# Kernel tuning notes

Measured on AMD Instinct MI355X. Metric: run time of the kernel, lower is better.

## Reference

```python
import jax, jax.numpy as jnp
import numpy as np
from jax import lax

# static config
P = 16          # patch_len
S = 8           # stride_base
MAX_OFF = 4.0


def setup_inputs() -> dict:
    key = jax.random.key(0)
    ks = jax.random.split(key, 7)
    B, L, N, A, D = 64, 512, 64, 64, 256
    x = jax.random.normal(ks[0], (B, L, N), dtype=jnp.float32)
    conv_w = jax.random.normal(ks[1], (32, N, 3), dtype=jnp.float32) * 0.05
    conv_b = jnp.zeros((32,), dtype=jnp.float32)
    lin_w = jax.random.normal(ks[2], (A, 32), dtype=jnp.float32) * 0.1
    lin_b = jnp.zeros((A,), dtype=jnp.float32)
    wp_w = jax.random.normal(ks[3], (D, P), dtype=jnp.float32) * 0.1
    wp_b = jnp.zeros((D,), dtype=jnp.float32)
    return {"x": x, "conv_w": conv_w, "conv_b": conv_b,
            "lin_w": lin_w, "lin_b": lin_b, "wp_w": wp_w, "wp_b": wp_b}


def _forward(x, conv_w, conv_b, lin_w, lin_b, wp_w, wp_b):
    B, L, N = x.shape
    A = lin_w.shape[0]
    D = wp_w.shape[0]
    z = jnp.transpose(x, (0, 2, 1))  # (B, N, L) -- channels = series

    # offset head: Conv1d(N->32, k=3, pad=1) -> ReLU -> global avg pool -> Linear(32->A)
    h = lax.conv_general_dilated(z, conv_w, window_strides=(1,),
                                 padding=[(1, 1)],
                                 dimension_numbers=("NCH", "OIH", "NCH"))
    h = jax.nn.relu(h + conv_b[None, :, None])      # (B, 32, L)
    pooled = jnp.mean(h, axis=-1)                    # (B, 32)
    delta = MAX_OFF * jnp.tanh(pooled @ lin_w.T + lin_b)  # (B, A)

    # sampling positions: anchor + offset + centered patch index, clamped to [0, L-1]
    anchors = jnp.arange(A, dtype=jnp.float32) * S
    pidx = jnp.arange(P, dtype=jnp.float32) - (P - 1) / 2.0
    xs = anchors[None, :, None] + delta[:, :, None] + pidx[None, None, :]  # (B, A, P)
    xs = jnp.clip(xs, 0.0, float(L - 1))

    # 1D bilinear gather (equivalent to grid_sample with y=0, border pad, align_corners=True)
    i0 = jnp.floor(xs).astype(jnp.int32)
    f = xs - i0.astype(xs.dtype)                     # (B, A, P)
    i1 = jnp.minimum(i0 + 1, L - 1)
    gather = jax.vmap(lambda zb, ib: zb[:, ib])      # (N,L),(A,P) -> (N,A,P)
    g0 = gather(z, i0)                               # (B, N, A, P)
    g1 = gather(z, i1)
    samp = g0 * (1.0 - f)[:, None] + g1 * f[:, None]  # (B, N, A, P)

    # patch projection W_P: (P -> D)
    out = jnp.einsum("bnap,dp->bnad", samp, wp_w) + wp_b  # (B, N, A, D)
    return out.reshape(B * N, A, D)


def reference(x, conv_w, conv_b, lin_w, lin_b, wp_w, wp_b):
    return _forward(x, conv_w, conv_b, lin_w, lin_b, wp_w, wp_b)
```

## Files before the change

kernel.cpp:

```cpp
#include <hip/hip_runtime.h>
#include <hip/hip_bf16.h>
#include <cmath>

#define BB 64
#define LL 512
#define NN 64
#define AA 64
#define PP 16
#define DD 256
#define MAX_OFF 4.0f
#define STRIDE_S 8

__global__ __launch_bounds__(256) void conv_pool_kernel(
    const float* __restrict__ x,
    const float* __restrict__ conv_w,
    const float* __restrict__ conv_b,
    float* __restrict__ pool_partial)
{
    const int c = blockIdx.x;
    const int b = blockIdx.y;
    const int t = threadIdx.x;

    __shared__ float4 wl[3 * 16 * 32];
    __shared__ float  xl[66 * 64];
    __shared__ float  red[8][32];

    for (int idx = t; idx < 1536; idx += 256) {
        int o  = idx & 31;
        int nv = (idx >> 5) & 15;
        int k  = idx >> 9;
        float4 v;
        v.x = conv_w[(o * 64 + nv * 4 + 0) * 3 + k];
        v.y = conv_w[(o * 64 + nv * 4 + 1) * 3 + k];
        v.z = conv_w[(o * 64 + nv * 4 + 2) * 3 + k];
        v.w = conv_w[(o * 64 + nv * 4 + 3) * 3 + k];
        wl[idx] = v;
    }

    const int base_row = c * 64 - 1;
    for (int idx = t; idx < 66 * 16; idx += 256) {
        int j  = idx >> 4;
        int nv = idx & 15;
        int row = base_row + j;
        float4 v = make_float4(0.f, 0.f, 0.f, 0.f);
        if (row >= 0 && row < LL)
            v = *reinterpret_cast<const float4*>(&x[((size_t)b * LL + row) * NN + nv * 4]);
        *reinterpret_cast<float4*>(&xl[j * 64 + nv * 4]) = v;
    }
    __syncthreads();

    const int o  = t & 31;
    const int lg = t >> 5;

    float s[8];
#pragma unroll
    for (int j = 0; j < 8; ++j) s[j] = 0.f;

#pragma unroll
    for (int nv = 0; nv < 16; ++nv) {
        float4 xv[10];
#pragma unroll
        for (int j = 0; j < 10; ++j)
            xv[j] = *reinterpret_cast<const float4*>(&xl[(lg * 8 + j) * 64 + nv * 4]);
#pragma unroll
        for (int k = 0; k < 3; ++k) {
            float4 w4 = wl[(k * 16 + nv) * 32 + o];
#pragma unroll
            for (int j = 0; j < 8; ++j) {
                s[j] = fmaf(xv[j + k].x, w4.x, s[j]);
                s[j] = fmaf(xv[j + k].y, w4.y, s[j]);
                s[j] = fmaf(xv[j + k].z, w4.z, s[j]);
                s[j] = fmaf(xv[j + k].w, w4.w, s[j]);
            }
        }
    }

    const float cb = conv_b[o];
    float part = 0.f;
#pragma unroll
    for (int j = 0; j < 8; ++j) part += fmaxf(s[j] + cb, 0.f);
    red[lg][o] = part;
    __syncthreads();

    if (t < 32) {
        float sum = 0.f;
#pragma unroll
        for (int g = 0; g < 8; ++g) sum += red[g][t];
        pool_partial[((size_t)b * 8 + c) * 32 + t] = sum;
    }
}

__global__ __launch_bounds__(64) void delta_kernel(
    const float* __restrict__ pool_partial,
    const float* __restrict__ lin_w,
    const float* __restrict__ lin_b,
    float* __restrict__ delta)
{
    const int b = blockIdx.x;
    const int t = threadIdx.x;
    __shared__ float pooled[32];

    if (t < 32) {
        float s = 0.f;
#pragma unroll
        for (int c = 0; c < 8; ++c) s += pool_partial[((size_t)b * 8 + c) * 32 + t];
        pooled[t] = s * (1.0f / 512.0f);
    }
    __syncthreads();

    float s = lin_b[t];
#pragma unroll
    for (int o = 0; o < 32; ++o) s = fmaf(pooled[o], lin_w[t * 32 + o], s);
    delta[b * AA + t] = MAX_OFF * tanhf(s);
}

#define XR_STRIDE 68

__global__ __launch_bounds__(256) void patch_proj_kernel(
    const float* __restrict__ x,
    const float* __restrict__ wp_w,
    const float* __restrict__ wp_b,
    const float* __restrict__ delta,
    float* __restrict__ out)
{
    const int a = blockIdx.x;
    const int b = blockIdx.y;
    const int t = threadIdx.x;

    __shared__ float xr[17 * XR_STRIDE];
    __shared__ float samp[64 * 16];

    const float dlt  = delta[b * AA + a];
    const float base = (float)(a * STRIDE_S) - 7.5f + dlt;
    const int   r0   = (int)floorf(base);

    for (int idx = t; idx < 17 * 16; idx += 256) {
        int j  = idx >> 4;
        int nv = idx & 15;
        int row = r0 + j;
        row = max(0, min(LL - 1, row));
        float4 v = *reinterpret_cast<const float4*>(&x[((size_t)b * LL + row) * NN + nv * 4]);
        *reinterpret_cast<float4*>(&xr[j * XR_STRIDE + nv * 4]) = v;
    }
    __syncthreads();

    {
        const int p = t & 15;
        float xs = base + (float)p;
        xs = fminf(fmaxf(xs, 0.f), (float)(LL - 1));
        int   i0 = (int)floorf(xs);
        float f  = xs - (float)i0;
        int   i1 = min(i0 + 1, LL - 1);
        const int j0 = i0 - r0;
        const int j1 = i1 - r0;
        const int nq = t >> 4;
#pragma unroll
        for (int i = 0; i < 4; ++i) {
            int n = nq + 16 * i;
            float g0 = xr[j0 * XR_STRIDE + n];
            float g1 = xr[j1 * XR_STRIDE + n];
            samp[n * 16 + p] = g0 + f * (g1 - g0);
        }
    }
    __syncthreads();

    const int dq = t & 63;
    const int ng = t >> 6;

    float w_[4][16];
#pragma unroll
    for (int r = 0; r < 4; ++r) {
#pragma unroll
        for (int pv = 0; pv < 4; ++pv) {
            float4 v = *reinterpret_cast<const float4*>(&wp_w[(dq * 4 + r) * 16 + pv * 4]);
            w_[r][pv * 4 + 0] = v.x;
            w_[r][pv * 4 + 1] = v.y;
            w_[r][pv * 4 + 2] = v.z;
            w_[r][pv * 4 + 3] = v.w;
        }
    }
    const float4 bias = *reinterpret_cast<const float4*>(&wp_b[dq * 4]);

#pragma unroll
    for (int i = 0; i < 16; ++i) {
        const int n = ng * 16 + i;
        const float4 s0 = *reinterpret_cast<const float4*>(&samp[n * 16 + 0]);
        const float4 s1 = *reinterpret_cast<const float4*>(&samp[n * 16 + 4]);
        const float4 s2 = *reinterpret_cast<const float4*>(&samp[n * 16 + 8]);
        const float4 s3 = *reinterpret_cast<const float4*>(&samp[n * 16 + 12]);
        float sp[16] = { s0.x, s0.y, s0.z, s0.w,  s1.x, s1.y, s1.z, s1.w,
                         s2.x, s2.y, s2.z, s2.w,  s3.x, s3.y, s3.z, s3.w };
        float acc0 = bias.x, acc1 = bias.y, acc2 = bias.z, acc3 = bias.w;
#pragma unroll
        for (int p = 0; p < 16; ++p) {
            const float s = sp[p];
            acc0 = fmaf(s, w_[0][p], acc0);
            acc1 = fmaf(s, w_[1][p], acc1);
            acc2 = fmaf(s, w_[2][p], acc2);
            acc3 = fmaf(s, w_[3][p], acc3);
        }
        const size_t row = ((size_t)(b * NN + n) * AA + a);
        float4 o4 = make_float4(acc0, acc1, acc2, acc3);
        *reinterpret_cast<float4*>(&out[row * DD + dq * 4]) = o4;
    }
}

extern "C" void kernel_launch(void* const* d_in, const int* in_sizes, int n_in,
                              void* d_out, int out_size, void* d_ws, size_t ws_size,
                              hipStream_t stream)
{
    const float* x      = (const float*)d_in[0];
    const float* conv_w = (const float*)d_in[1];
    const float* conv_b = (const float*)d_in[2];
    const float* lin_w  = (const float*)d_in[3];
    const float* lin_b  = (const float*)d_in[4];
    const float* wp_w   = (const float*)d_in[5];
    const float* wp_b   = (const float*)d_in[6];
    float* out = (float*)d_out;

    float* pool_partial = (float*)d_ws;
    float* delta        = pool_partial + 16384;

    conv_pool_kernel<<<dim3(8, BB), 256, 0, stream>>>(x, conv_w, conv_b, pool_partial);
    delta_kernel<<<BB, 64, 0, stream>>>(pool_partial, lin_w, lin_b, delta);
    patch_proj_kernel<<<dim3(AA, BB), 256, 0, stream>>>(x, wp_w, wp_b, delta, out);
}
```

Baseline: 74.08 us.

## Use bf16 MFMA for patch projection with zero-padded K

Replaces the scalar FP32 FMA patch projection with a bf16 MFMA 16x16x32 matrix multiply. Sampled values and projection weights are converted to bf16 in shared memory, with K padded from 16 to 32 using zeros. Output is now written as scalar stores strided across d instead of float4 stores. This lowers precision to bf16 and may hurt store coalescing, while the kernel is likely bound by output writes anyway.

```diff
diff --git a/kernel.cpp b/kernel.cpp
--- a/kernel.cpp
+++ b/kernel.cpp
@@ -10,6 +10,15 @@
 #define DD 256
 #define MAX_OFF 4.0f
 #define STRIDE_S 8
+
+typedef __attribute__((ext_vector_type(8))) short short8_t;
+typedef __attribute__((ext_vector_type(4))) float float4_t;
+
+static __device__ __forceinline__ unsigned short f2bf(float x) {
+    union { float f; unsigned u; } v; v.f = x;
+    unsigned r = (v.u + 0x7FFFu + ((v.u >> 16) & 1u)) >> 16;
+    return (unsigned short)r;
+}
 
 __global__ __launch_bounds__(256) void conv_pool_kernel(
     const float* __restrict__ x,
@@ -115,6 +124,8 @@
 }
 
 #define XR_STRIDE 68
+#define SA_STRIDE 40
+#define BW_STRIDE 24
 
 __global__ __launch_bounds__(256) void patch_proj_kernel(
     const float* __restrict__ x,
@@ -126,9 +137,14 @@
     const int a = blockIdx.x;
     const int b = blockIdx.y;
     const int t = threadIdx.x;
-
-    __shared__ float xr[17 * XR_STRIDE];
-    __shared__ float samp[64 * 16];
+    const int lane = t & 63;
+    const int w  = t >> 6;
+    const int lg = lane >> 4;
+    const int lr = lane & 15;
+
+    __shared__ float          xr[17 * XR_STRIDE];
+    __shared__ unsigned short sampA[64 * SA_STRIDE];
+    __shared__ unsigned short bw[256 * BW_STRIDE];
 
     const float dlt  = delta[b * AA + a];
     const float base = (float)(a * STRIDE_S) - 7.5f + dlt;
@@ -137,71 +153,90 @@
     for (int idx = t; idx < 17 * 16; idx += 256) {
         int j  = idx >> 4;
         int nv = idx & 15;
-        int row = r0 + j;
-        row = max(0, min(LL - 1, row));
+        int row = max(0, min(LL - 1, r0 + j));
         float4 v = *reinterpret_cast<const float4*>(&x[((size_t)b * LL + row) * NN + nv * 4]);
         *reinterpret_cast<float4*>(&xr[j * XR_STRIDE + nv * 4]) = v;
     }
+    for (int idx = t; idx < 256 * 8; idx += 256) {
+        int d  = idx >> 3;
+        int pp = idx & 7;
+        float2 v = *reinterpret_cast<const float2*>(&wp_w[d * 16 + pp * 2]);
+        unsigned pk = (unsigned)f2bf(v.x) | ((unsigned)f2bf(v.y) << 16);
+        *reinterpret_cast<unsigned*>(&bw[d * BW_STRIDE + pp * 2]) = pk;
+    }
+    for (int idx = t; idx < 64 * 8; idx += 256) {
+        int n  = idx >> 3;
+        int ww = idx & 7;
+        reinterpret_cast<unsigned*>(&sampA[n * SA_STRIDE])[8 + ww] = 0u;
+    }
     __syncthreads();
 
     {
-        const int p = t & 15;
-        float xs = base + (float)p;
-        xs = fminf(fmaxf(xs, 0.f), (float)(LL - 1));
-        int   i0 = (int)floorf(xs);
-        float f  = xs - (float)i0;
-        int   i1 = min(i0 + 1, LL - 1);
-        const int j0 = i0 - r0;
-        const int j1 = i1 - r0;
-        const int nq = t >> 4;
-#pragma unroll
-        for (int i = 0; i < 4; ++i) {
-            int n = nq + 16 * i;
-            float g0 = xr[j0 * XR_STRIDE + n];
-            float g1 = xr[j1 * XR_STRIDE + n];
-            samp[n * 16 + p] = g0 + f * (g1 - g0);
-        }
-    }
-    __syncthreads();
-
-    const int dq = t & 63;
-    const int ng = t >> 6;
-
-    float w_[4][16];
-#pragma unroll
-    for (int r = 0; r < 4; ++r) {
-#pragma unroll
-        for (int pv = 0; pv < 4; ++pv) {
-            float4 v = *reinterpret_cast<const float4*>(&wp_w[(dq * 4 + r) * 16 + pv * 4]);
-            w_[r][pv * 4 + 0] = v.x;
-            w_[r][pv * 4 + 1] = v.y;
-            w_[r][pv * 4 + 2] = v.z;
-            w_[r][pv * 4 + 3] = v.w;
-        }
-    }
-    const float4 bias = *reinterpret_cast<const float4*>(&wp_b[dq * 4]);
-
-#pragma unroll
-    for (int i = 0; i < 16; ++i) {
-        const int n = ng * 16 + i;
-        const float4 s0 = *reinterpret_cast<const float4*>(&samp[n * 16 + 0]);
-        const float4 s1 = *reinterpret_cast<const float4*>(&samp[n * 16 + 4]);
-        const float4 s2 = *reinterpret_cast<const float4*>(&samp[n * 16 + 8]);
-        const float4 s3 = *reinterpret_cast<const float4*>(&samp[n * 16 + 12]);
-        float sp[16] = { s0.x, s0.y, s0.z, s0.w,  s1.x, s1.y, s1.z, s1.w,
-                         s2.x, s2.y, s2.z, s2.w,  s3.x, s3.y, s3.z, s3.w };
-        float acc0 = bias.x, acc1 = bias.y, acc2 = bias.z, acc3 = bias.w;
-#pragma unroll
-        for (int p = 0; p < 16; ++p) {
-            const float s = sp[p];
-            acc0 = fmaf(s, w_[0][p], acc0);
-            acc1 = fmaf(s, w_[1][p], acc1);
-            acc2 = fmaf(s, w_[2][p], acc2);
-            acc3 = fmaf(s, w_[3][p], acc3);
-        }
-        const size_t row = ((size_t)(b * NN + n) * AA + a);
-        float4 o4 = make_float4(acc0, acc1, acc2, acc3);
-        *reinterpret_cast<float4*>(&out[row * DD + dq * 4]) = o4;
+        const int pp  = t & 7;
+        const int nr0 = t >> 3;
+        float f_[2]; int j0_[2], j1_[2];
+#pragma unroll
+        for (int q = 0; q < 2; ++q) {
+            int p = pp * 2 + q;
+            float xs = base + (float)p;
+            xs = fminf(fmaxf(xs, 0.f), (float)(LL - 1));
+            int i0 = (int)floorf(xs);
+            f_[q]  = xs - (float)i0;
+            j0_[q] = i0 - r0;
+            j1_[q] = min(i0 + 1, LL - 1) - r0;
+        }
+#pragma unroll
+        for (int h = 0; h < 2; ++h) {
+            int n = nr0 + 32 * h;
+            unsigned pk = 0;
+#pragma unroll
+            for (int q = 0; q < 2; ++q) {
+                float g0 = xr[j0_[q] * XR_STRIDE + n];
+                float g1 = xr[j1_[q] * XR_STRIDE + n];
+                float s  = g0 + f_[q] * (g1 - g0);
+                pk |= (unsigned)f2bf(s) << (16 * q);
+            }
+            *reinterpret_cast<unsigned*>(&sampA[n * SA_STRIDE + pp * 2]) = pk;
+        }
+    }
+
+    short8_t bfrag[4];
+    float4_t acc[4][4];
+#pragma unroll
+    for (int i = 0; i < 4; ++i) {
+        int d = (w * 4 + i) * 16 + lr;
+        bfrag[i] = *reinterpret_cast<const short8_t*>(&bw[d * BW_STRIDE + (lg & 1) * 8]);
+        float bias = wp_b[d];
+        float4_t c4 = {bias, bias, bias, bias};
+#pragma unroll
+        for (int s = 0; s < 4; ++s) acc[s][i] = c4;
+    }
+    __syncthreads();
+
+    short8_t afrag[4];
+#pragma unroll
+    for (int s = 0; s < 4; ++s)
+        afrag[s] = *reinterpret_cast<const short8_t*>(
+            &sampA[(s * 16 + lr) * SA_STRIDE + lg * 8]);
+
+#pragma unroll
+    for (int s = 0; s < 4; ++s)
+#pragma unroll
+        for (int i = 0; i < 4; ++i)
+            acc[s][i] = __builtin_amdgcn_mfma_f32_16x16x32_bf16(
+                afrag[s], bfrag[i], acc[s][i], 0, 0, 0);
+
+    const size_t obase = ((size_t)(b * NN) * AA + a) * DD + (size_t)w * 64 + lr;
+#pragma unroll
+    for (int s = 0; s < 4; ++s) {
+#pragma unroll
+        for (int j = 0; j < 4; ++j) {
+            const int n = s * 16 + lg * 4 + j;
+            const size_t rowoff = obase + (size_t)n * (AA * DD);
+#pragma unroll
+            for (int i = 0; i < 4; ++i)
+                out[rowoff + i * 16] = acc[s][i][j];
+        }
     }
 }
 
```

New measurement: 66.47 us. 10.3% less time.
